# Kernel optimization log

Hardware: AMD Instinct MI355X
Metric: run time of the kernel (lower is better)

## Reference

```python
import jax, jax.numpy as jnp
import numpy as np

M = 200000   # number of lane candidates
N = 5000     # number of obstacles
NUM_NODE = 150
FEAT = 4


def setup_inputs() -> dict:
    key = jax.random.key(0)
    k1, k2, k3 = jax.random.split(key, 3)
    lane_features = jax.random.normal(k1, (M, NUM_NODE, FEAT), dtype=jnp.float32)
    obs_pos = jax.random.normal(k2, (N, 2), dtype=jnp.float32)
    same_obs_mask = jnp.sort(jax.random.randint(k3, (M, 1), 0, N), axis=0)
    return {"lane_features": lane_features, "obs_pos": obs_pos,
            "same_obs_mask": same_obs_mask}


def reference(lane_features, obs_pos, same_obs_mask):
    lf = lane_features.astype(jnp.float32)          # (M, 150, 4)
    m = lf.shape[0]
    ar = jnp.arange(m)

    # BroadcastObstaclesToLanes: the serial masked-write loop is exactly a gather.
    rep = obs_pos[same_obs_mask[:, 0]].astype(jnp.float32)   # (M, 2)

    # FindClosestNodeFromLineToPoint: interior nodes [1:-1], xy only.
    nodes = lf[:, 1:-1, :2]                          # (M, 148, 2)
    dists = jnp.sum((nodes - rep[:, None, :]) ** 2, axis=-1)  # (M, 148)
    min_idx = jnp.argmin(dists, axis=1) + 1          # (M,), in [1, 148]

    # FindClosestLineSegmentFromLineToPoint (note: distances use all 4 feats,
    # faithfully matching line_nodes[..., :] in the original).
    min_node = lf[ar, min_idx]                       # (M, 4)
    node_prev = lf[ar, min_idx - 1]
    node_next = lf[ar, min_idx + 1]
    dist_prev = jnp.sum((node_prev - min_node) ** 2, axis=1)
    dist_next = jnp.sum((node_next - min_node) ** 2, axis=1)
    min_idx_2nd = jnp.where(dist_next < dist_prev, min_idx + 1, min_idx - 1)
    idx_before = jnp.minimum(min_idx, min_idx_2nd)
    idx_after = jnp.maximum(min_idx, min_idx_2nd)

    # PointToLineProjection on the xy of the chosen segment endpoints.
    seg_s = lf[ar, idx_before, :2]                   # (M, 2)
    seg_e = lf[ar, idx_after, :2]                    # (M, 2)
    line_vec = seg_e - seg_s
    mag = jnp.sqrt(jnp.sum(line_vec ** 2, axis=1, keepdims=True))
    unit = line_vec / mag
    proj_mag = jnp.sum((rep - seg_s) * unit, axis=1, keepdims=True)
    proj_pt = seg_s + proj_mag * unit                # (M, 2)

    indices = jnp.stack([idx_before, idx_after], axis=1)  # (M, 2)
    return proj_pt, indices, rep
```

## Files before the change

kernel.cpp:

```cpp
#include <hip/hip_runtime.h>
#include <math.h>

static constexpr int M_ROWS   = 200000;
static constexpr int NUM_NODE = 150;
static constexpr int ROWS_PER_BLOCK = 4;

__global__ __launch_bounds__(256) void obstacle_to_lane_kernel(
    const float* __restrict__ lf,
    const float* __restrict__ obs_pos,
    const int*   __restrict__ mask,
    float*       __restrict__ out)
{
    const int wave = threadIdx.x >> 6;
    const int lane = threadIdx.x & 63;
    const int m = blockIdx.x * ROWS_PER_BLOCK + wave;
    if (m >= M_ROWS) return;

    const float* row = lf + (size_t)m * (NUM_NODE * 4);

    const int obs_idx = mask[m];
    const float rx = obs_pos[2 * obs_idx];
    const float ry = obs_pos[2 * obs_idx + 1];

    float best_d = INFINITY;
    int   best_j = 1 << 30;
    #pragma unroll
    for (int r = 0; r < 3; ++r) {
        const int j = 1 + lane + r * 64;
        if (j <= NUM_NODE - 2) {
            const float4 n = *reinterpret_cast<const float4*>(row + 4 * j);
            const float dx = __fsub_rn(n.x, rx);
            const float dy = __fsub_rn(n.y, ry);
            const float d  = __fadd_rn(__fmul_rn(dx, dx), __fmul_rn(dy, dy));
            if (d < best_d) { best_d = d; best_j = j; }
        }
    }
    #pragma unroll
    for (int off = 32; off > 0; off >>= 1) {
        const float od = __shfl_down(best_d, off, 64);
        const int   oj = __shfl_down(best_j, off, 64);
        if (od < best_d || (od == best_d && oj < best_j)) { best_d = od; best_j = oj; }
    }
    const int min_idx = __shfl(best_j, 0, 64);

    if (lane == 0) {
        const float4 a = *reinterpret_cast<const float4*>(row + 4 * (min_idx - 1));
        const float4 c = *reinterpret_cast<const float4*>(row + 4 * min_idx);
        const float4 b = *reinterpret_cast<const float4*>(row + 4 * (min_idx + 1));

        float t, s;
        t = __fsub_rn(a.x, c.x); s = __fmul_rn(t, t);
        t = __fsub_rn(a.y, c.y); s = __fadd_rn(s, __fmul_rn(t, t));
        t = __fsub_rn(a.z, c.z); s = __fadd_rn(s, __fmul_rn(t, t));
        t = __fsub_rn(a.w, c.w); s = __fadd_rn(s, __fmul_rn(t, t));
        const float dist_prev = s;
        t = __fsub_rn(b.x, c.x); s = __fmul_rn(t, t);
        t = __fsub_rn(b.y, c.y); s = __fadd_rn(s, __fmul_rn(t, t));
        t = __fsub_rn(b.z, c.z); s = __fadd_rn(s, __fmul_rn(t, t));
        t = __fsub_rn(b.w, c.w); s = __fadd_rn(s, __fmul_rn(t, t));
        const float dist_next = s;

        float sx, sy, ex, ey;
        int ib;
        if (dist_next < dist_prev) {
            ib = min_idx;     sx = c.x; sy = c.y; ex = b.x; ey = b.y;
        } else {
            ib = min_idx - 1; sx = a.x; sy = a.y; ex = c.x; ey = c.y;
        }

        const float lvx = __fsub_rn(ex, sx);
        const float lvy = __fsub_rn(ey, sy);
        const float mag = __fsqrt_rn(__fadd_rn(__fmul_rn(lvx, lvx), __fmul_rn(lvy, lvy)));
        const float ux  = __fdiv_rn(lvx, mag);
        const float uy  = __fdiv_rn(lvy, mag);
        const float pm  = __fadd_rn(__fmul_rn(__fsub_rn(rx, sx), ux),
                                    __fmul_rn(__fsub_rn(ry, sy), uy));
        const float px  = __fadd_rn(sx, __fmul_rn(pm, ux));
        const float py  = __fadd_rn(sy, __fmul_rn(pm, uy));

        float* o_proj = out + 2 * (size_t)m;
        o_proj[0] = px; o_proj[1] = py;
        float* o_idx = out + 2 * (size_t)M_ROWS + 2 * (size_t)m;
        o_idx[0] = (float)ib; o_idx[1] = (float)(ib + 1);
        float* o_rep = out + 4 * (size_t)M_ROWS + 2 * (size_t)m;
        o_rep[0] = rx; o_rep[1] = ry;
    }
}

extern "C" void kernel_launch(void* const* d_in, const int* in_sizes, int n_in,
                              void* d_out, int out_size, void* d_ws, size_t ws_size,
                              hipStream_t stream) {
    const float* lf      = (const float*)d_in[0];
    const float* obs_pos = (const float*)d_in[1];
    const int*   mask    = (const int*)d_in[2];
    float*       out     = (float*)d_out;

    const int grid = (M_ROWS + ROWS_PER_BLOCK - 1) / ROWS_PER_BLOCK;
    hipLaunchKernelGGL(obstacle_to_lane_kernel, dim3(grid), dim3(256), 0, stream,
                       lf, obs_pos, mask, out);
}
```

Measured before the change: 612.0 us.

## Use persistent grid-stride waves with register prefetch of next lane row

Replaces the one-row-per-wave launch with a fixed grid of 2048 blocks whose waves stride over rows. Each wave loads the next row's nodes and mask into registers while it computes the current row, so memory latency overlaps with the reduction. The argmin reduction now packs distance bits and index into one 64-bit key, which halves the shuffles per step. This adds register pressure and a loop-carried dependency, and it relies on the distances being non-negative so that the bit-pattern ordering matches the float ordering.

After: 618.5 us. No clear change (+1.1%).

```diff
diff --git a/kernel.cpp b/kernel.cpp
--- a/kernel.cpp
+++ b/kernel.cpp
@@ -3,87 +3,120 @@
 
 static constexpr int M_ROWS   = 200000;
 static constexpr int NUM_NODE = 150;
-static constexpr int ROWS_PER_BLOCK = 4;
+static constexpr int TPB      = 256;
+static constexpr int NBLOCKS  = 2048;
+static constexpr int NWAVES   = NBLOCKS * (TPB / 64);
 
-__global__ __launch_bounds__(256) void obstacle_to_lane_kernel(
+__global__ __launch_bounds__(TPB, 4) void obstacle_to_lane_kernel(
     const float* __restrict__ lf,
-    const float* __restrict__ obs_pos,
+    const float* __restrict__ obs,
     const int*   __restrict__ mask,
     float*       __restrict__ out)
 {
-    const int wave = threadIdx.x >> 6;
     const int lane = threadIdx.x & 63;
-    const int m = blockIdx.x * ROWS_PER_BLOCK + wave;
-    if (m >= M_ROWS) return;
+    const int gw   = (int)((blockIdx.x * TPB + threadIdx.x) >> 6);
 
-    const float* row = lf + (size_t)m * (NUM_NODE * 4);
+    const int  j0 = 1 + lane;
+    const int  j1 = 65 + lane;
+    const bool v2 = (129 + lane) <= (NUM_NODE - 2);
+    const int  j2 = v2 ? (129 + lane) : (NUM_NODE - 2);
 
-    const int obs_idx = mask[m];
-    const float rx = obs_pos[2 * obs_idx];
-    const float ry = obs_pos[2 * obs_idx + 1];
+    int r = gw;
+    if (r >= M_ROWS) return;
 
-    float best_d = INFINITY;
-    int   best_j = 1 << 30;
-    #pragma unroll
-    for (int r = 0; r < 3; ++r) {
-        const int j = 1 + lane + r * 64;
-        if (j <= NUM_NODE - 2) {
-            const float4 n = *reinterpret_cast<const float4*>(row + 4 * j);
-            const float dx = __fsub_rn(n.x, rx);
-            const float dy = __fsub_rn(n.y, ry);
-            const float d  = __fadd_rn(__fmul_rn(dx, dx), __fmul_rn(dy, dy));
-            if (d < best_d) { best_d = d; best_j = j; }
-        }
-    }
-    #pragma unroll
-    for (int off = 32; off > 0; off >>= 1) {
-        const float od = __shfl_down(best_d, off, 64);
-        const int   oj = __shfl_down(best_j, off, 64);
-        if (od < best_d || (od == best_d && oj < best_j)) { best_d = od; best_j = oj; }
-    }
-    const int min_idx = __shfl(best_j, 0, 64);
+    const float* rp = lf + (size_t)r * (NUM_NODE * 4);
+    int    nmask = mask[__builtin_amdgcn_readfirstlane(r)];
+    float4 n0 = *reinterpret_cast<const float4*>(rp + 4 * j0);
+    float4 n1 = *reinterpret_cast<const float4*>(rp + 4 * j1);
+    float4 n2 = *reinterpret_cast<const float4*>(rp + 4 * j2);
 
-    if (lane == 0) {
-        const float4 a = *reinterpret_cast<const float4*>(row + 4 * (min_idx - 1));
-        const float4 c = *reinterpret_cast<const float4*>(row + 4 * min_idx);
-        const float4 b = *reinterpret_cast<const float4*>(row + 4 * (min_idx + 1));
+    for (;;) {
+        const int rc = r;
+        r += NWAVES;
+        const bool more = (r < M_ROWS);
 
-        float t, s;
-        t = __fsub_rn(a.x, c.x); s = __fmul_rn(t, t);
-        t = __fsub_rn(a.y, c.y); s = __fadd_rn(s, __fmul_rn(t, t));
-        t = __fsub_rn(a.z, c.z); s = __fadd_rn(s, __fmul_rn(t, t));
-        t = __fsub_rn(a.w, c.w); s = __fadd_rn(s, __fmul_rn(t, t));
-        const float dist_prev = s;
-        t = __fsub_rn(b.x, c.x); s = __fmul_rn(t, t);
-        t = __fsub_rn(b.y, c.y); s = __fadd_rn(s, __fmul_rn(t, t));
-        t = __fsub_rn(b.z, c.z); s = __fadd_rn(s, __fmul_rn(t, t));
-        t = __fsub_rn(b.w, c.w); s = __fadd_rn(s, __fmul_rn(t, t));
-        const float dist_next = s;
+        const int    mcur = nmask;
+        const float4 a0 = n0, a1 = n1, a2 = n2;
 
-        float sx, sy, ex, ey;
-        int ib;
-        if (dist_next < dist_prev) {
-            ib = min_idx;     sx = c.x; sy = c.y; ex = b.x; ey = b.y;
-        } else {
-            ib = min_idx - 1; sx = a.x; sy = a.y; ex = c.x; ey = c.y;
+        if (more) {
+            const float* np = lf + (size_t)r * (NUM_NODE * 4);
+            nmask = mask[__builtin_amdgcn_readfirstlane(r)];
+            n0 = *reinterpret_cast<const float4*>(np + 4 * j0);
+            n1 = *reinterpret_cast<const float4*>(np + 4 * j1);
+            n2 = *reinterpret_cast<const float4*>(np + 4 * j2);
         }
 
-        const float lvx = __fsub_rn(ex, sx);
-        const float lvy = __fsub_rn(ey, sy);
-        const float mag = __fsqrt_rn(__fadd_rn(__fmul_rn(lvx, lvx), __fmul_rn(lvy, lvy)));
-        const float ux  = __fdiv_rn(lvx, mag);
-        const float uy  = __fdiv_rn(lvy, mag);
-        const float pm  = __fadd_rn(__fmul_rn(__fsub_rn(rx, sx), ux),
-                                    __fmul_rn(__fsub_rn(ry, sy), uy));
-        const float px  = __fadd_rn(sx, __fmul_rn(pm, ux));
-        const float py  = __fadd_rn(sy, __fmul_rn(pm, uy));
+        const float rx = obs[2 * mcur];
+        const float ry = obs[2 * mcur + 1];
 
-        float* o_proj = out + 2 * (size_t)m;
-        o_proj[0] = px; o_proj[1] = py;
-        float* o_idx = out + 2 * (size_t)M_ROWS + 2 * (size_t)m;
-        o_idx[0] = (float)ib; o_idx[1] = (float)(ib + 1);
-        float* o_rep = out + 4 * (size_t)M_ROWS + 2 * (size_t)m;
-        o_rep[0] = rx; o_rep[1] = ry;
+        unsigned long long key;
+        {
+            float dx, dy, d;
+            dx = __fsub_rn(a0.x, rx); dy = __fsub_rn(a0.y, ry);
+            d  = __fadd_rn(__fmul_rn(dx, dx), __fmul_rn(dy, dy));
+            key = ((unsigned long long)__float_as_uint(d) << 32) | (unsigned)j0;
+
+            dx = __fsub_rn(a1.x, rx); dy = __fsub_rn(a1.y, ry);
+            d  = __fadd_rn(__fmul_rn(dx, dx), __fmul_rn(dy, dy));
+            unsigned long long k1 = ((unsigned long long)__float_as_uint(d) << 32) | (unsigned)j1;
+            if (k1 < key) key = k1;
+
+            dx = __fsub_rn(a2.x, rx); dy = __fsub_rn(a2.y, ry);
+            d  = __fadd_rn(__fmul_rn(dx, dx), __fmul_rn(dy, dy));
+            unsigned long long k2 = ((unsigned long long)__float_as_uint(d) << 32) | (unsigned)j2;
+            if (v2 && k2 < key) key = k2;
+        }
+        #pragma unroll
+        for (int off = 32; off > 0; off >>= 1) {
+            const unsigned long long o = __shfl_down(key, off, 64);
+            if (o < key) key = o;
+        }
+        const int min_idx = (int)(unsigned)__shfl(key, 0, 64);
+
+        if (lane == 0) {
+            const float* rowc = lf + (size_t)rc * (NUM_NODE * 4);
+            const float4 a = *reinterpret_cast<const float4*>(rowc + 4 * (min_idx - 1));
+            const float4 c = *reinterpret_cast<const float4*>(rowc + 4 * min_idx);
+            const float4 b = *reinterpret_cast<const float4*>(rowc + 4 * (min_idx + 1));
+
+            float t, s;
+            t = __fsub_rn(a.x, c.x); s = __fmul_rn(t, t);
+            t = __fsub_rn(a.y, c.y); s = __fadd_rn(s, __fmul_rn(t, t));
+            t = __fsub_rn(a.z, c.z); s = __fadd_rn(s, __fmul_rn(t, t));
+            t = __fsub_rn(a.w, c.w); s = __fadd_rn(s, __fmul_rn(t, t));
+            const float dist_prev = s;
+            t = __fsub_rn(b.x, c.x); s = __fmul_rn(t, t);
+            t = __fsub_rn(b.y, c.y); s = __fadd_rn(s, __fmul_rn(t, t));
+            t = __fsub_rn(b.z, c.z); s = __fadd_rn(s, __fmul_rn(t, t));
+            t = __fsub_rn(b.w, c.w); s = __fadd_rn(s, __fmul_rn(t, t));
+            const float dist_next = s;
+
+            float sx, sy, ex, ey; int ib;
+            if (dist_next < dist_prev) {
+                ib = min_idx;     sx = c.x; sy = c.y; ex = b.x; ey = b.y;
+            } else {
+                ib = min_idx - 1; sx = a.x; sy = a.y; ex = c.x; ey = c.y;
+            }
+
+            const float lvx = __fsub_rn(ex, sx);
+            const float lvy = __fsub_rn(ey, sy);
+            const float mag = __fsqrt_rn(__fadd_rn(__fmul_rn(lvx, lvx), __fmul_rn(lvy, lvy)));
+            const float ux  = __fdiv_rn(lvx, mag);
+            const float uy  = __fdiv_rn(lvy, mag);
+            const float pm  = __fadd_rn(__fmul_rn(__fsub_rn(rx, sx), ux),
+                                        __fmul_rn(__fsub_rn(ry, sy), uy));
+            const float px  = __fadd_rn(sx, __fmul_rn(pm, ux));
+            const float py  = __fadd_rn(sy, __fmul_rn(pm, uy));
+
+            float* o_proj = out + 2 * (size_t)rc;
+            o_proj[0] = px; o_proj[1] = py;
+            float* o_idx = out + 2 * (size_t)M_ROWS + 2 * (size_t)rc;
+            o_idx[0] = (float)ib; o_idx[1] = (float)(ib + 1);
+            float* o_rep = out + 4 * (size_t)M_ROWS + 2 * (size_t)rc;
+            o_rep[0] = rx; o_rep[1] = ry;
+        }
+
+        if (!more) break;
     }
 }
 
@@ -95,7 +128,6 @@
     const int*   mask    = (const int*)d_in[2];
     float*       out     = (float*)d_out;
 
-    const int grid = (M_ROWS + ROWS_PER_BLOCK - 1) / ROWS_PER_BLOCK;
-    hipLaunchKernelGGL(obstacle_to_lane_kernel, dim3(grid), dim3(256), 0, stream,
+    hipLaunchKernelGGL(obstacle_to_lane_kernel, dim3(NBLOCKS), dim3(TPB), 0, stream,
                        lf, obs_pos, mask, out);
 }
```
